# Kernel optimization log

Hardware: AMD Instinct MI355X
Metric: run time of the kernel (lower is better)

Reference implementation:

```python
import jax, jax.numpy as jnp
import numpy as np
import math

B, S, HID = 1, 2048, 4096
HQ, HKV, D = 32, 8, 128
G = HQ // HKV          # GQA group size
OBS, W, SINK = 128, 32, 2
THETA = 500000.0
TOP_FRAC, MID_SPARSITY, LOW_FRAC = 0.05, 0.7, 0.20
K_KEEP = int(math.ceil((1.0 - MID_SPARSITY) * D))  # elements kept per level-1 token


def _rope(x):
    # x: [B, H, S, D]; standard Llama rotary embedding
    half = D // 2
    inv_freq = 1.0 / (THETA ** (jnp.arange(half, dtype=jnp.float32) / half))
    ang = jnp.arange(S, dtype=jnp.float32)[:, None] * inv_freq[None, :]  # [S, half]
    cos = jnp.concatenate([jnp.cos(ang), jnp.cos(ang)], axis=-1)  # [S, D]
    sin = jnp.concatenate([jnp.sin(ang), jnp.sin(ang)], axis=-1)
    x1, x2 = x[..., :half], x[..., half:]
    rot = jnp.concatenate([-x2, x1], axis=-1)
    return x * cos[None, None] + rot * sin[None, None]


def _topk_mask(x):
    # keep the K_KEEP largest-magnitude elements of each length-D token vector
    a = jnp.abs(x)
    thr = jnp.sort(a, axis=-1)[..., D - K_KEEP]
    return a >= thr[..., None]


def setup_inputs() -> dict:
    key = jax.random.key(0)
    ks = jax.random.split(key, 5)
    sc = HID ** -0.5
    return {
        "hidden_states": jax.random.normal(ks[0], (B, S, HID), dtype=jnp.float32),
        "wq": jax.random.normal(ks[1], (HID, HQ * D), dtype=jnp.float32) * sc,
        "wk": jax.random.normal(ks[2], (HID, HKV * D), dtype=jnp.float32) * sc,
        "wv": jax.random.normal(ks[3], (HID, HKV * D), dtype=jnp.float32) * sc,
        "wo": jax.random.normal(ks[4], (HQ * D, HID), dtype=jnp.float32) * sc,
    }


def reference(hidden_states, wq, wk, wv, wo):
    scale = 1.0 / math.sqrt(D)
    q = (hidden_states @ wq).reshape(B, S, HQ, D).transpose(0, 2, 1, 3)   # [B,HQ,S,D]
    k = (hidden_states @ wk).reshape(B, S, HKV, D).transpose(0, 2, 1, 3)  # [B,HKV,S,D]
    v = (hidden_states @ wv).reshape(B, S, HKV, D).transpose(0, 2, 1, 3)
    q, k = _rope(q), _rope(k)

    # --- observation-window GQA attention (grouped queries vs all keys) ---
    obs_q = q[:, :, S - OBS:, :].reshape(B, HKV, G, OBS, D)
    s_obs = jnp.einsum('bhgqd,bhkd->bhgqk', obs_q, k) * scale
    obs_causal = jnp.arange(S)[None, :] <= (S - OBS + jnp.arange(OBS))[:, None]  # [OBS,S]
    s_obs = jnp.where(obs_causal[None, None, None], s_obs, -jnp.inf)
    aw_kv = jax.nn.softmax(s_obs.astype(jnp.float32), axis=-1).mean(axis=2)  # [B,HKV,OBS,S]

    # per-token importance, normalized by how many obs queries observed each key
    counts = jnp.minimum(OBS, S - jnp.arange(S)).astype(jnp.float32)
    imp = aw_kv.sum(axis=2) / counts[None, None, :]  # [B,HKV,S]

    # --- global thresholds over the compressible region -> 3 sparsity levels ---
    imp_c = imp[:, :, :S - W].reshape(-1)
    t_high = jnp.quantile(imp_c, 1.0 - TOP_FRAC)
    t_low = jnp.quantile(imp_c, LOW_FRAC)
    level = jnp.where(imp >= t_high, 0, jnp.where(imp < t_low, 2, 1))
    pos = jnp.arange(S)
    dense_pos = (pos >= S - W) | (pos < SINK)     # recent window + sinks stay dense
    level = jnp.where(dense_pos[None, None, :], 0, level)

    keep_k = jnp.where((level == 0)[..., None], True, (level == 1)[..., None] & _topk_mask(k))
    keep_v = jnp.where((level == 0)[..., None], True, (level == 1)[..., None] & _topk_mask(v))
    k_sp = k * keep_k
    v_sp = v * keep_v
    evicted = level == 2

    # --- causal GQA attention over the sparsified KV cache ---
    q_g = q.reshape(B, HKV, G, S, D)
    s = jnp.einsum('bhgqd,bhkd->bhgqk', q_g, k_sp) * scale
    causal = jnp.tril(jnp.ones((S, S), dtype=bool))
    allow = causal[None, None, None] & (~evicted)[:, :, None, None, :]
    s = jnp.where(allow, s, -jnp.inf)
    p = jax.nn.softmax(s.astype(jnp.float32), axis=-1).astype(v_sp.dtype)
    o = jnp.einsum('bhgqk,bhkd->bhgqd', p, v_sp)
    o = o.reshape(B, HQ, S, D).transpose(0, 2, 1, 3).reshape(B, S, HQ * D)
    return o @ wo
```

## Files before the change

### kernel.cpp

```cpp
#include <hip/hip_runtime.h>
#include <hip/hip_bf16.h>
#include <math.h>

#define S_    2048
#define HID_  4096
#define HQ_   32
#define HKV_  8
#define D_    128
#define G_    4
#define OBS_  128
#define W_    32
#define NKV_  1024
#define NQ_   4096
#define KLD_  2048
#define SCALE_ 0.08838834764831845f
#define THR_IDX_ 89
#define NC_   16128

typedef __attribute__((ext_vector_type(4))) float f32x4;
typedef __attribute__((ext_vector_type(8))) short s16x8;
typedef __attribute__((ext_vector_type(8))) unsigned short u16x8;
typedef __attribute__((ext_vector_type(4))) unsigned short u16x4;
typedef unsigned short ushort_t;

struct TermPtrs { const ushort_t* a[6]; const ushort_t* b[6]; };

__device__ __forceinline__ unsigned short f2bf(float x) {
  union { float f; unsigned u; } v; v.f = x;
  unsigned r = v.u + 0x7FFFu + ((v.u >> 16) & 1u);
  return (unsigned short)(r >> 16);
}
__device__ __forceinline__ float bf2f(unsigned short b) {
  union { unsigned u; float f; } v; v.u = ((unsigned)b) << 16;
  return v.f;
}
__device__ __forceinline__ void gload_lds16(const void* g, void* l) {
  __builtin_amdgcn_global_load_lds((const __attribute__((address_space(1))) unsigned int*)g,
                                   (__attribute__((address_space(3))) unsigned int*)l, 16, 0, 0);
}
__device__ __forceinline__ void term_sel(const TermPtrs& P, int tt,
                                         const ushort_t*& As, const ushort_t*& Bs) {
  switch (tt) {
    case 0: As = P.a[0]; Bs = P.b[0]; break;
    case 1: As = P.a[1]; Bs = P.b[1]; break;
    case 2: As = P.a[2]; Bs = P.b[2]; break;
    case 3: As = P.a[3]; Bs = P.b[3]; break;
    case 4: As = P.a[4]; Bs = P.b[4]; break;
    default: As = P.a[5]; Bs = P.b[5]; break;
  }
}
__device__ __forceinline__ void xcd_bmbn(int& bm, int& bn) {
  int nplane = gridDim.x * gridDim.y;
  int l = blockIdx.y * gridDim.x + blockIdx.x;
  int v = (l & 7) * (nplane >> 3) + (l >> 3);
  bm = v / gridDim.x;
  bn = v - bm * gridDim.x;
}

__global__ __launch_bounds__(256) void split3_kernel(const float* __restrict__ src,
                                                     ushort_t* __restrict__ d0,
                                                     ushort_t* __restrict__ d1,
                                                     ushort_t* __restrict__ d2, int n4) {
  int idx = blockIdx.x * 256 + threadIdx.x;
  if (idx >= n4) return;
  float4 v = ((const float4*)src)[idx];
  u16x4 o0, o1, o2;
  float xs[4] = {v.x, v.y, v.z, v.w};
#pragma unroll
  for (int e = 0; e < 4; ++e) {
    float x = xs[e];
    unsigned short b0 = f2bf(x);
    float r = x - bf2f(b0);
    unsigned short b1 = f2bf(r);
    o0[e] = b0; o1[e] = b1; o2[e] = f2bf(r - bf2f(b1));
  }
  *(u16x4*)(d0 + (size_t)idx * 4) = o0;
  *(u16x4*)(d1 + (size_t)idx * 4) = o1;
  *(u16x4*)(d2 + (size_t)idx * 4) = o2;
}

__global__ __launch_bounds__(256) void splitT_kernel(const float* __restrict__ src, int N,
                                                     ushort_t* __restrict__ t0,
                                                     ushort_t* __restrict__ t1,
                                                     ushort_t* __restrict__ t2) {
  __shared__ float tile[64][65];
  const int t = threadIdx.x;
  const int n0 = blockIdx.x * 64, k0 = blockIdx.y * 64;
#pragma unroll
  for (int i = 0; i < 16; ++i) {
    int idx = i * 256 + t;
    int r = idx >> 6, c = idx & 63;
    tile[r][c] = src[(size_t)(k0 + r) * N + n0 + c];
  }
  __syncthreads();
#pragma unroll
  for (int i = 0; i < 16; ++i) {
    int idx = i * 256 + t;
    int n = idx >> 6, kk = idx & 63;
    float x = tile[kk][n];
    unsigned short b0 = f2bf(x);
    size_t o = (size_t)(n0 + n) * HID_ + k0 + kk;
    t0[o] = b0;
    if (t1) {
      float r = x - bf2f(b0);
      unsigned short b1 = f2bf(r);
      t1[o] = b1;
      t2[o] = f2bf(r - bf2f(b1));
    }
  }
}

template<int TPZ>
__global__ __launch_bounds__(256) void gemm6(TermPtrs P, float* __restrict__ Cbase,
                                             int M, int N, int K) {
  __shared__ ushort_t lds[2 * 128 * 64];
  const int t = threadIdx.x;
  const int wave = t >> 6, lane = t & 63;
  const int lc = lane & 15, lg = lane >> 4;
  int bm, bn;
  xcd_bmbn(bm, bn);
  const int z = blockIdx.z;
  const int wm = wave >> 1, wn = wave & 1;
  const int srow = t >> 3, schunk = t & 7;
  float* C = Cbase + (size_t)z * M * N;

  f32x4 acc[4][4];
#pragma unroll
  for (int fi = 0; fi < 4; ++fi)
#pragma unroll
    for (int fj = 0; fj < 4; ++fj) acc[fi][fj] = 0.f;

  for (int tt = z * TPZ; tt < z * TPZ + TPZ; ++tt) {
    const ushort_t *As, *Bs;
    term_sel(P, tt, As, Bs);
    for (int kb = 0; kb < K / 64; ++kb) {
      __syncthreads();
#pragma unroll
      for (int g = 0; g < 4; ++g) {
        int row = g * 32 + srow;
        int sw = schunk ^ (row & 7);
        gload_lds16(As + (size_t)(bm * 128 + row) * K + kb * 64 + sw * 8,
                    lds + g * 2048 + wave * 512);
        gload_lds16(Bs + (size_t)(bn * 128 + row) * K + kb * 64 + sw * 8,
                    lds + 8192 + g * 2048 + wave * 512);
      }
      __syncthreads();
#pragma unroll
      for (int ks = 0; ks < 2; ++ks) {
        s16x8 af[4], bf[4];
#pragma unroll
        for (int f = 0; f < 4; ++f) {
          int ra = wm * 64 + f * 16 + lc;
          af[f] = *(const s16x8*)(lds + ra * 64 + (((ks * 4 + lg) ^ (ra & 7)) * 8));
          int rb = wn * 64 + f * 16 + lc;
          bf[f] = *(const s16x8*)(lds + 8192 + rb * 64 + (((ks * 4 + lg) ^ (rb & 7)) * 8));
        }
#pragma unroll
        for (int fi = 0; fi < 4; ++fi)
#pragma unroll
          for (int fj = 0; fj < 4; ++fj)
            acc[fi][fj] = __builtin_amdgcn_mfma_f32_16x16x32_bf16(af[fi], bf[fj], acc[fi][fj], 0, 0, 0);
      }
    }
  }
#pragma unroll
  for (int fi = 0; fi < 4; ++fi)
#pragma unroll
    for (int fj = 0; fj < 4; ++fj)
#pragma unroll
      for (int r = 0; r < 4; ++r)
        C[(size_t)(bm * 128 + wm * 64 + fi * 16 + lg * 4 + r) * N +
          bn * 128 + wn * 64 + fj * 16 + lc] = acc[fi][fj][r];
}

__global__ __launch_bounds__(256) void gemm1(const ushort_t* __restrict__ A,
                                             const ushort_t* __restrict__ B,
                                             float* __restrict__ Cbase,
                                             int M, int N, int K, int KSTEPS) {
  __shared__ ushort_t lds[2 * 128 * 64];
  const int t = threadIdx.x;
  const int wave = t >> 6, lane = t & 63;
  const int lc = lane & 15, lg = lane >> 4;
  int bm, bn;
  xcd_bmbn(bm, bn);
  const int z = blockIdx.z;
  const int wm = wave >> 1, wn = wave & 1;
  const int srow = t >> 3, schunk = t & 7;
  float* C = Cbase + (size_t)z * M * N;

  f32x4 acc[4][4];
#pragma unroll
  for (int fi = 0; fi < 4; ++fi)
#pragma unroll
    for (int fj = 0; fj < 4; ++fj) acc[fi][fj] = 0.f;

  for (int kb = z * KSTEPS; kb < z * KSTEPS + KSTEPS; ++kb) {
    __syncthreads();
#pragma unroll
    for (int g = 0; g < 4; ++g) {
      int row = g * 32 + srow;
      int sw = schunk ^ (row & 7);
      size_t co = kb * 64 + sw * 8;
      gload_lds16(A + (size_t)(bm * 128 + row) * K + co, lds + g * 2048 + wave * 512);
      gload_lds16(B + (size_t)(bn * 128 + row) * K + co, lds + 8192 + g * 2048 + wave * 512);
    }
    __syncthreads();
#pragma unroll
    for (int ks = 0; ks < 2; ++ks) {
      s16x8 af[4], bf[4];
#pragma unroll
      for (int f = 0; f < 4; ++f) {
        int ra = wm * 64 + f * 16 + lc;
        af[f] = *(const s16x8*)(lds + ra * 64 + (((ks * 4 + lg) ^ (ra & 7)) * 8));
        int rb = wn * 64 + f * 16 + lc;
        bf[f] = *(const s16x8*)(lds + 8192 + rb * 64 + (((ks * 4 + lg) ^ (rb & 7)) * 8));
      }
#pragma unroll
      for (int fi = 0; fi < 4; ++fi)
#pragma unroll
        for (int fj = 0; fj < 4; ++fj)
          acc[fi][fj] = __builtin_amdgcn_mfma_f32_16x16x32_bf16(af[fi], bf[fj], acc[fi][fj], 0, 0, 0);
    }
  }
#pragma unroll
  for (int fi = 0; fi < 4; ++fi)
#pragma unroll
    for (int fj = 0; fj < 4; ++fj)
#pragma unroll
      for (int r = 0; r < 4; ++r)
        C[(size_t)(bm * 128 + wm * 64 + fi * 16 + lg * 4 + r) * N +
          bn * 128 + wn * 64 + fj * 16 + lc] = acc[fi][fj][r];
}

__global__ __launch_bounds__(256) void gemm6k(TermPtrs P, float* __restrict__ Cp, int N) {
  __shared__ ushort_t lds[2 * 128 * 64];
  const int t = threadIdx.x;
  const int wave = t >> 6, lane = t & 63;
  const int lc = lane & 15, lg = lane >> 4;
  const int bn = blockIdx.x, z = blockIdx.z;
  const int wm = wave >> 1, wn = wave & 1;
  const int srow = t >> 3, schunk = t & 7;
  float* C = Cp + (size_t)z * 128 * N;

  f32x4 acc[4][4];
#pragma unroll
  for (int fi = 0; fi < 4; ++fi)
#pragma unroll
    for (int fj = 0; fj < 4; ++fj) acc[fi][fj] = 0.f;

  for (int tt = 0; tt < 6; ++tt) {
    const ushort_t *As, *Bs;
    term_sel(P, tt, As, Bs);
    for (int kb = z * 8; kb < z * 8 + 8; ++kb) {
      __syncthreads();
#pragma unroll
      for (int g = 0; g < 4; ++g) {
        int row = g * 32 + srow;
        int sw = schunk ^ (row & 7);
        gload_lds16(As + (size_t)row * HID_ + kb * 64 + sw * 8,
                    lds + g * 2048 + wave * 512);
        gload_lds16(Bs + (size_t)(bn * 128 + row) * HID_ + kb * 64 + sw * 8,
                    lds + 8192 + g * 2048 + wave * 512);
      }
      __syncthreads();
#pragma unroll
      for (int ks = 0; ks < 2; ++ks) {
        s16x8 af[4], bf[4];
#pragma unroll
        for (int f = 0; f < 4; ++f) {
          int ra = wm * 64 + f * 16 + lc;
          af[f] = *(const s16x8*)(lds + ra * 64 + (((ks * 4 + lg) ^ (ra & 7)) * 8));
          int rb = wn * 64 + f * 16 + lc;
          bf[f] = *(const s16x8*)(lds + 8192 + rb * 64 + (((ks * 4 + lg) ^ (rb & 7)) * 8));
        }
#pragma unroll
        for (int fi = 0; fi < 4; ++fi)
#pragma unroll
          for (int fj = 0; fj < 4; ++fj)
            acc[fi][fj] = __builtin_amdgcn_mfma_f32_16x16x32_bf16(af[fi], bf[fj], acc[fi][fj], 0, 0, 0);
      }
    }
  }
#pragma unroll
  for (int fi = 0; fi < 4; ++fi)
#pragma unroll
    for (int fj = 0; fj < 4; ++fj)
#pragma unroll
      for (int r = 0; r < 4; ++r)
        C[(size_t)(wm * 64 + fi * 16 + lg * 4 + r) * N +
          bn * 128 + wn * 64 + fj * 16 + lc] = acc[fi][fj][r];
}

__global__ __launch_bounds__(256) void gemm6z(TermPtrs P, float* __restrict__ Cg) {
  __shared__ ushort_t lds[2 * 128 * 64];
  const int t = threadIdx.x;
  const int wave = t >> 6, lane = t & 63;
  const int lc = lane & 15, lg = lane >> 4;
  const int bm = blockIdx.y, bn = blockIdx.x, z = blockIdx.z;
  const int wm = wave >> 1, wn = wave & 1;
  const int srow = t >> 3, schunk = t & 7;
  const size_t Aoff = (size_t)z * 512 * 128;
  const size_t Boff = (size_t)z * 2048 * 128;
  float* C = Cg + (size_t)z * 512 * 2048;

  f32x4 acc[4][4];
#pragma unroll
  for (int fi = 0; fi < 4; ++fi)
#pragma unroll
    for (int fj = 0; fj < 4; ++fj) acc[fi][fj] = 0.f;

  for (int tt = 0; tt < 6; ++tt) {
    const ushort_t *As, *Bs;
    term_sel(P, tt, As, Bs);
    As += Aoff; Bs += Boff;
    for (int kb = 0; kb < 2; ++kb) {
      __syncthreads();
#pragma unroll
      for (int g = 0; g < 4; ++g) {
        int row = g * 32 + srow;
        int sw = schunk ^ (row & 7);
        gload_lds16(As + (size_t)(bm * 128 + row) * 128 + kb * 64 + sw * 8,
                    lds + g * 2048 + wave * 512);
        gload_lds16(Bs + (size_t)(bn * 128 + row) * 128 + kb * 64 + sw * 8,
                    lds + 8192 + g * 2048 + wave * 512);
      }
      __syncthreads();
#pragma unroll
      for (int ks = 0; ks < 2; ++ks) {
        s16x8 af[4], bf[4];
#pragma unroll
        for (int f = 0; f < 4; ++f) {
          int ra = wm * 64 + f * 16 + lc;
          af[f] = *(const s16x8*)(lds + ra * 64 + (((ks * 4 + lg) ^ (ra & 7)) * 8));
          int rb = wn * 64 + f * 16 + lc;
          bf[f] = *(const s16x8*)(lds + 8192 + rb * 64 + (((ks * 4 + lg) ^ (rb & 7)) * 8));
        }
#pragma unroll
        for (int fi = 0; fi < 4; ++fi)
#pragma unroll
          for (int fj = 0; fj < 4; ++fj)
            acc[fi][fj] = __builtin_amdgcn_mfma_f32_16x16x32_bf16(af[fi], bf[fj], acc[fi][fj], 0, 0, 0);
      }
    }
  }
#pragma unroll
  for (int fi = 0; fi < 4; ++fi)
#pragma unroll
    for (int fj = 0; fj < 4; ++fj)
#pragma unroll
      for (int r = 0; r < 4; ++r)
        C[(size_t)(bm * 128 + wm * 64 + fi * 16 + lg * 4 + r) * 2048 +
          bn * 128 + wn * 64 + fj * 16 + lc] = acc[fi][fj][r];
}

__global__ void reduce3_kernel(const float* __restrict__ p, float* __restrict__ out, int n4) {
  int idx = blockIdx.x * 256 + threadIdx.x;
  if (idx >= n4) return;
  const size_t n = (size_t)n4 * 4;
  float4 a = ((const float4*)p)[idx];
  float4 b = ((const float4*)(p + n))[idx];
  float4 c = ((const float4*)(p + 2 * n))[idx];
  float4 o;
  o.x = a.x + b.x + c.x; o.y = a.y + b.y + c.y;
  o.z = a.z + b.z + c.z; o.w = a.w + b.w + c.w;
  ((float4*)out)[idx] = o;
}
__global__ void reduce2_kernel(const float* __restrict__ p, float* __restrict__ out, int n4) {
  int idx = blockIdx.x * 256 + threadIdx.x;
  if (idx >= n4) return;
  const size_t n = (size_t)n4 * 4;
  float4 a = ((const float4*)p)[idx];
  float4 b = ((const float4*)(p + n))[idx];
  float4 o;
  o.x = a.x + b.x; o.y = a.y + b.y; o.z = a.z + b.z; o.w = a.w + b.w;
  ((float4*)out)[idx] = o;
}

__global__ void freq_kernel(float* __restrict__ invf) {
  int j = threadIdx.x;
  if (j < 64) invf[j] = (float)(1.0 / pow(500000.0, (double)j / 64.0));
}

__global__ __launch_bounds__(256) void qobs_fuse(const float* __restrict__ qpart,
                                                 const float* __restrict__ invf,
                                                 ushort_t* __restrict__ q0,
                                                 ushort_t* __restrict__ q1,
                                                 ushort_t* __restrict__ q2) {
  int idx = blockIdx.x * 256 + threadIdx.x;
  int j = idx & 63;
  int hq = (idx >> 6) & 31;
  int i = idx >> 11;
  size_t base = (size_t)i * NQ_ + hq * 128 + j;
  float x1 = 0.f, x2 = 0.f;
#pragma unroll
  for (int z = 0; z < 8; ++z) {
    x1 += qpart[(size_t)z * OBS_ * NQ_ + base];
    x2 += qpart[(size_t)z * OBS_ * NQ_ + base + 64];
  }
  float ang = (float)(S_ - OBS_ + i) * invf[j];
  float sn, cs; sincosf(ang, &sn, &cs);
  float o1 = x1 * cs - x2 * sn;
  float o2 = x2 * cs + x1 * sn;
  int hk = hq >> 2, g = hq & 3;
  size_t o = (size_t)hk * 65536 + (size_t)(g * 128 + i) * 128 + j;
  float ys[2] = {o1, o2};
#pragma unroll
  for (int e = 0; e < 2; ++e) {
    float x = ys[e];
    unsigned short b0 = f2bf(x);
    float r = x - bf2f(b0);
    unsigned short b1 = f2bf(r);
    q0[o + e * 64] = b0; q1[o + e * 64] = b1; q2[o + e * 64] = f2bf(r - bf2f(b1));
  }
}

__global__ __launch_bounds__(256) void ropekv_splitk(float* __restrict__ kvf,
                                                     const float* __restrict__ invf,
                                                     ushort_t* __restrict__ k0,
                                                     ushort_t* __restrict__ k1,
                                                     ushort_t* __restrict__ k2) {
  int idx = blockIdx.x * 256 + threadIdx.x;
  int j = idx & 63;
  int h = (idx >> 6) & 7;
  int s = idx >> 9;
  size_t base = (size_t)s * KLD_ + h * 128 + j;
  float x1 = kvf[base], x2 = kvf[base + 64];
  float ang = (float)s * invf[j];
  float sn, cs; sincosf(ang, &sn, &cs);
  float o1 = x1 * cs - x2 * sn;
  float o2 = x2 * cs + x1 * sn;
  kvf[base] = o1; kvf[base + 64] = o2;
  size_t o = (size_t)h * 262144 + (size_t)s * 128 + j;
  float ys[2] = {o1, o2};
#pragma unroll
  for (int e = 0; e < 2; ++e) {
    float x = ys[e];
    unsigned short b0 = f2bf(x);
    float r = x - bf2f(b0);
    unsigned short b1 = f2bf(r);
    k0[o + e * 64] = b0; k1[o + e * 64] = b1; k2[o + e * 64] = f2bf(r - bf2f(b1));
  }
}

__global__ __launch_bounds__(256) void rope_q_fuse(const float* __restrict__ qp,
                                                   const float* __restrict__ invf,
                                                   ushort_t* __restrict__ qb16) {
  int idx = blockIdx.x * 256 + threadIdx.x;
  int j = idx & 63;
  int h = (idx >> 6) & 31;
  int s = idx >> 11;
  size_t base = (size_t)s * NQ_ + h * 128 + j;
  const size_t zs = (size_t)S_ * NQ_;
  float x1 = qp[base] + qp[base + zs];
  float x2 = qp[base + 64] + qp[base + 64 + zs];
  float ang = (float)s * invf[j];
  float sn, cs; sincosf(ang, &sn, &cs);
  qb16[base] = f2bf(x1 * cs - x2 * sn);
  qb16[base + 64] = f2bf(x2 * cs + x1 * sn);
}

__global__ __launch_bounds__(256) void rowstat_kernel(const float* __restrict__ s,
                                                      float* __restrict__ mx,
                                                      float* __restrict__ dinv) {
  const int row = blockIdx.x * 4 + (threadIdx.x >> 6);
  const int lane = threadIdx.x & 63;
  const int i = row & 127;
  const int jmax = S_ - OBS_ + i;
  const float* sp = s + (size_t)row * S_;
  float vals[32];
  float m = -INFINITY;
#pragma unroll
  for (int c = 0; c < 8; ++c) {
    int j0 = c * 256 + lane * 4;
    float4 v = *(const float4*)(sp + j0);
    float e0 = (j0 + 0 <= jmax) ? v.x * SCALE_ : -INFINITY;
    float e1 = (j0 + 1 <= jmax) ? v.y * SCALE_ : -INFINITY;
    float e2 = (j0 + 2 <= jmax) ? v.z * SCALE_ : -INFINITY;
    float e3 = (j0 + 3 <= jmax) ? v.w * SCALE_ : -INFINITY;
    vals[c * 4 + 0] = e0; vals[c * 4 + 1] = e1; vals[c * 4 + 2] = e2; vals[c * 4 + 3] = e3;
    m = fmaxf(m, fmaxf(fmaxf(e0, e1), fmaxf(e2, e3)));
  }
#pragma unroll
  for (int off = 1; off < 64; off <<= 1) m = fmaxf(m, __shfl_xor(m, off, 64));
  float ssum = 0.f;
#pragma unroll
  for (int c = 0; c < 32; ++c) ssum += expf(vals[c] - m);
#pragma unroll
  for (int off = 1; off < 64; off <<= 1) ssum += __shfl_xor(ssum, off, 64);
  if (lane == 0) { mx[row] = m; dinv[row] = 1.0f / ssum; }
}

__global__ __launch_bounds__(256) void colsum_part(const float* __restrict__ s,
                                                   const float* __restrict__ mx,
                                                   const float* __restrict__ dinv,
                                                   float* __restrict__ part) {
  __shared__ float mxl[64], dvl[64];
  const int jt = blockIdx.x, hk = blockIdx.y, rc = blockIdx.z;
  const int t = threadIdx.x;
  if (t < 64) {
    mxl[t] = mx[hk * 512 + rc * 64 + t];
    dvl[t] = dinv[hk * 512 + rc * 64 + t];
  }
  __syncthreads();
  const int j = jt * 256 + t;
  const float* sp = s + ((size_t)hk * 512 + rc * 64) * S_ + j;
  float acc = 0.f;
  for (int rr = 0; rr < 64; ++rr) {
    int i = (rc * 64 + rr) & 127;
    if (j <= S_ - OBS_ + i)
      acc += expf(sp[(size_t)rr * S_] * SCALE_ - mxl[rr]) * dvl[rr];
  }
  part[((size_t)rc * 8 + hk) * S_ + j] = acc;
}

__global__ void colsum_fin(const float* __restrict__ part, float* __restrict__ imp) {
  int idx = blockIdx.x * 256 + threadIdx.x;
  int hk = idx >> 11, j = idx & 2047;
  float acc = 0.f;
#pragma unroll
  for (int rc = 0; rc < 8; ++rc) acc += part[((size_t)rc * 8 + hk) * S_ + j];
  float cnt = (float)min(OBS_, S_ - j);
  imp[idx] = acc * 0.25f / cnt;
}

__global__ __launch_bounds__(1024) void radix_all(const float* __restrict__ imp,
                                                  float* __restrict__ thr) {
  __shared__ unsigned hist[4][256];
  __shared__ unsigned pfx_s[4], need_s[4];
  const int t = threadIdx.x;
  if (t < 4) {
    pfx_s[t] = 0u;
    need_s[t] = (t == 0) ? 3225u : (t == 1) ? 3226u : (t == 2) ? 15320u : 15321u;
  }
  __syncthreads();
  for (int pass = 0; pass < 4; ++pass) {
    ((unsigned*)hist)[t] = 0u;
    __syncthreads();
    int shift = 24 - pass * 8;
    for (int idx = t; idx < NC_; idx += 1024) {
      int h = idx / (S_ - W_), j = idx - h * (S_ - W_);
      union { float f; unsigned u; } cv; cv.f = imp[h * S_ + j];
      unsigned u = cv.u;
#pragma unroll
      for (int q = 0; q < 4; ++q) {
        bool m = (pass == 0) || ((u >> (shift + 8)) == (pfx_s[q] >> (shift + 8)));
        if (m) atomicAdd(&hist[q][(u >> shift) & 255u], 1u);
      }
    }
    __syncthreads();
    if (t < 4) {
      unsigned need = need_s[t], cum = 0, pfx = pfx_s[t];
      for (int d = 0; d < 256; ++d) {
        unsigned c = hist[t][d];
        if (cum + c > need) { pfx |= ((unsigned)d) << shift; need_s[t] = need - cum; break; }
        cum += c;
      }
      pfx_s[t] = pfx;
    }
    __syncthreads();
  }
  if (t == 0) {
    union { unsigned u; float f; } c0, c1, c2, c3;
    c0.u = pfx_s[0]; c1.u = pfx_s[1]; c2.u = pfx_s[2]; c3.u = pfx_s[3];
    double fl = 0.2 * (double)(NC_ - 1) - 3225.0;
    double fh = 0.95 * (double)(NC_ - 1) - 15320.0;
    thr[0] = (float)((double)c2.f + ((double)c3.f - (double)c2.f) * fh);
    thr[1] = (float)((double)c0.f + ((double)c1.f - (double)c0.f) * fl);
  }
}

__global__ __launch_bounds__(128) void sparsify_kernel(const float* __restrict__ kv,
                                                       const float* __restrict__ imp,
                                                       const float* __restrict__ thr,
                                                       ushort_t* __restrict__ ksp,
                                                       ushort_t* __restrict__ vsp,
                                                       float* __restrict__ ebias) {
  const int b = blockIdx.x;
  const int j = b >> 3;
  const int h = b & 7;
  const int t = threadIdx.x;
  float ipv = imp[h * S_ + j];
  bool dense = (j >= S_ - W_) || (j < 2);
  int lvl = dense ? 0 : ((ipv >= thr[0]) ? 0 : ((ipv < thr[1]) ? 2 : 1));
  if (t == 0) ebias[h * S_ + j] = (lvl == 2) ? -INFINITY : 0.0f;
  __shared__ float av[128];
  __shared__ float thv;
  size_t base_in = (size_t)j * KLD_ + h * D_;
  size_t base_out = (size_t)j * NKV_ + h * D_;
  float kvv = kv[base_in + t];
  av[t] = fabsf(kvv);
  __syncthreads();
  {
    float at = av[t]; int cnt = 0;
    for (int m = 0; m < 128; ++m) { float am = av[m]; cnt += (am < at) || (am == at && m < t); }
    if (cnt == THR_IDX_) thv = at;
  }
  __syncthreads();
  {
    bool keep = (lvl == 0) || (lvl == 1 && fabsf(kvv) >= thv);
    ksp[base_out + t] = f2bf(keep ? kvv : 0.0f);
  }
  __syncthreads();
  float vvv = kv[base_in + 1024 + t];
  av[t] = fabsf(vvv);
  __syncthreads();
  {
    float at = av[t]; int cnt = 0;
    for (int m = 0; m < 128; ++m) { float am = av[m]; cnt += (am < at) || (am == at && m < t); }
    if (cnt == THR_IDX_) thv = at;
  }
  __syncthreads();
  {
    bool keep = (lvl == 0) || (lvl == 1 && fabsf(vvv) >= thv);
    vsp[base_out + t] = f2bf(keep ? vvv : 0.0f);
  }
}

__global__ __launch_bounds__(256) void vtrans_kernel(const ushort_t* __restrict__ vsp,
                                                     ushort_t* __restrict__ vspT) {
  __shared__ ushort_t tl[64][136];
  const int jt = blockIdx.x;
  const int hk = blockIdx.y;
  const int t = threadIdx.x;
#pragma unroll
  for (int i = 0; i < 4; ++i) {
    int idx = i * 256 + t;
    int j = idx >> 4, c = idx & 15;
    *(u16x8*)&tl[j][c * 8] = *(const u16x8*)(vsp + (size_t)(jt * 64 + j) * NKV_ + hk * 128 + c * 8);
  }
  __syncthreads();
  int d = t >> 1, j0 = (t & 1) * 32;
#pragma unroll
  for (int jj = 0; jj < 4; ++jj) {
    u16x8 v;
#pragma unroll
    for (int e = 0; e < 8; ++e) v[e] = tl[j0 + jj * 8 + e][d];
    *(u16x8*)(vspT + ((size_t)hk * 128 + d) * S_ + jt * 64 + j0 + jj * 8) = v;
  }
}

#define SPAD_ 66
__global__ __launch_bounds__(256) void attn_kernel(const ushort_t* __restrict__ qbp,
                                                   const ushort_t* __restrict__ ksp,
                                                   const ushort_t* __restrict__ vspT,
                                                   const float* __restrict__ ebias,
                                                   ushort_t* __restrict__ ob16) {
  __shared__ ushort_t k_lds[64 * 128];
  __shared__ ushort_t vT_lds[128 * 64];
  __shared__ float s_lds[4][16][SPAD_];
  const int b = blockIdx.x;
  const int xcd = b & 7;
  const int idx = b >> 3;
  const int h = xcd * 4 + (idx >> 4);
  const int p = idx & 15;
  const int hk = h >> 2;
  const int t = threadIdx.x;
  const int w = t >> 6, lane = t & 63;
  const int lc = lane & 15, lg = lane >> 4;

  const ushort_t* kbase = ksp + hk * D_;
  const ushort_t* vbase = vspT + (size_t)hk * D_ * S_;

  for (int strip = 0; strip < 2; ++strip) {
    const int qb = (strip == 0) ? p : 31 - p;
    const int q0 = qb * 64 + w * 16;
    s16x8 qfrag[4];
#pragma unroll
    for (int db = 0; db < 4; ++db)
      qfrag[db] = *(const s16x8*)(qbp + (size_t)(q0 + lc) * NQ_ + h * D_ + db * 32 + lg * 8);

    f32x4 o[8];
#pragma unroll
    for (int n = 0; n < 8; ++n) o[n] = 0.f;
    float mr[4] = {-INFINITY, -INFINITY, -INFINITY, -INFINITY};
    float lr[4] = {0.f, 0.f, 0.f, 0.f};

    const int ntj = qb + 1;
    for (int tj = 0; tj < ntj; ++tj) {
      const int j0 = tj * 64;
      __syncthreads();
#pragma unroll
      for (int i = 0; i < 4; ++i) {
        int slot = i * 256 + w * 64 + lane;
        int row = slot >> 4, c = slot & 15;
        const ushort_t* gp = kbase + (size_t)(j0 + row) * NKV_ + ((c ^ (row & 7)) * 8);
        gload_lds16(gp, &k_lds[(i * 256 + w * 64) * 8]);
      }
#pragma unroll
      for (int i = 0; i < 4; ++i) {
        int slot = i * 256 + w * 64 + lane;
        int d = slot >> 3, c = slot & 7;
        const ushort_t* gp = vbase + (size_t)d * S_ + j0 + ((c ^ (d & 7)) * 8);
        gload_lds16(gp, &vT_lds[(i * 256 + w * 64) * 8]);
      }
      __syncthreads();

      f32x4 sfr[4];
#pragma unroll
      for (int js = 0; js < 4; ++js) sfr[js] = 0.f;
#pragma unroll
      for (int js = 0; js < 4; ++js) {
        int row = js * 16 + lc;
#pragma unroll
        for (int db = 0; db < 4; ++db) {
          s16x8 kf = *(const s16x8*)&k_lds[row * 128 + (((db * 4 + lg) ^ (lc & 7)) * 8)];
          sfr[js] = __builtin_amdgcn_mfma_f32_16x16x32_bf16(qfrag[db], kf, sfr[js], 0, 0, 0);
        }
      }
      float eb[4];
#pragma unroll
      for (int js = 0; js < 4; ++js) eb[js] = ebias[hk * S_ + j0 + js * 16 + lc];

      const bool diag = (tj == qb);
      float sclv[4];
#pragma unroll
      for (int r = 0; r < 4; ++r) {
        float sv[4];
#pragma unroll
        for (int js = 0; js < 4; ++js) sv[js] = sfr[js][r] * SCALE_ + eb[js];
        if (diag) {
          int qrow = w * 16 + lg * 4 + r;
#pragma unroll
          for (int js = 0; js < 4; ++js)
            if (js * 16 + lc > qrow) sv[js] = -INFINITY;
        }
        float tm = fmaxf(fmaxf(sv[0], sv[1]), fmaxf(sv[2], sv[3]));
#pragma unroll
        for (int off = 1; off < 16; off <<= 1) tm = fmaxf(tm, __shfl_xor(tm, off, 64));
        float mnew = fmaxf(mr[r], tm);
        float scl = __expf(mr[r] - mnew);
        float ps = 0.f;
#pragma unroll
        for (int js = 0; js < 4; ++js) {
          float e = __expf(sv[js] - mnew);
          s_lds[w][lg * 4 + r][js * 16 + lc] = e;
          ps += e;
        }
#pragma unroll
        for (int off = 1; off < 16; off <<= 1) ps += __shfl_xor(ps, off, 64);
        lr[r] = lr[r] * scl + ps;
        mr[r] = mnew;
        sclv[r] = scl;
      }
#pragma unroll
      for (int n = 0; n < 8; ++n) {
        f32x4 ov = o[n];
#pragma unroll
        for (int r = 0; r < 4; ++r) ov[r] *= sclv[r];
        o[n] = ov;
      }
      asm volatile("s_waitcnt lgkmcnt(0)" ::: "memory");
      s16x8 pa[2];
#pragma unroll
      for (int ks = 0; ks < 2; ++ks) {
        float pv[8];
        *(f32x4*)&pv[0] = *(const f32x4*)&s_lds[w][lc][ks * 32 + lg * 8];
        *(f32x4*)&pv[4] = *(const f32x4*)&s_lds[w][lc][ks * 32 + lg * 8 + 4];
        s16x8 pk;
#pragma unroll
        for (int e = 0; e < 8; ++e) pk[e] = (short)f2bf(pv[e]);
        pa[ks] = pk;
      }
#pragma unroll
      for (int n = 0; n < 8; ++n) {
        int d = n * 16 + lc;
#pragma unroll
        for (int ks = 0; ks < 2; ++ks) {
          s16x8 vf = *(const s16x8*)&vT_lds[d * 64 + (((ks * 4 + lg) ^ (lc & 7)) * 8)];
          o[n] = __builtin_amdgcn_mfma_f32_16x16x32_bf16(pa[ks], vf, o[n], 0, 0, 0);
        }
      }
    }
#pragma unroll
    for (int r = 0; r < 4; ++r) {
      float rinv = 1.0f / lr[r];
      int row = q0 + lg * 4 + r;
#pragma unroll
      for (int n = 0; n < 8; ++n)
        ob16[(size_t)row * NQ_ + h * D_ + n * 16 + lc] = f2bf(o[n][r] * rinv);
    }
  }
}

extern "C" void kernel_launch(void* const* d_in, const int* in_sizes, int n_in,
                              void* d_out, int out_size, void* d_ws, size_t ws_size,
                              hipStream_t stream) {
  (void)in_sizes; (void)n_in; (void)out_size; (void)ws_size;
  const float* hid = (const float*)d_in[0];
  const float* wq  = (const float*)d_in[1];
  const float* wk  = (const float*)d_in[2];
  const float* wv  = (const float*)d_in[3];
  const float* wo  = (const float*)d_in[4];
  float* out = (float*)d_out;
  char* ws = (char*)d_ws;
  const size_t MB = 1ull << 20;

  ushort_t* h0     = (ushort_t*)(ws + 0 * MB);
  ushort_t* h1     = (ushort_t*)(ws + 16 * MB);
  ushort_t* h2     = (ushort_t*)(ws + 32 * MB);
  ushort_t* wq0T   = (ushort_t*)(ws + 48 * MB);
  ushort_t* wq1T   = (ushort_t*)(ws + 80 * MB);
  ushort_t* wq2T   = (ushort_t*)(ws + 112 * MB);
  ushort_t* wkv0T  = (ushort_t*)(ws + 144 * MB);
  ushort_t* wkv1T  = (ushort_t*)(ws + 160 * MB);
  ushort_t* wkv2T  = (ushort_t*)(ws + 176 * MB);
  float*    qpart  = (float*)(ws + 192 * MB);
  float*    kvf    = (float*)(ws + 192 * MB);
  float*    kvp    = (float*)(ws + 80 * MB);
  float*    qp2    = (float*)(ws + 80 * MB);
  ushort_t* qb16   = (ushort_t*)(ws + 16 * MB);
  ushort_t* kb0    = (ushort_t*)(ws + 32 * MB);
  ushort_t* kb1    = (ushort_t*)(ws + 36 * MB);
  ushort_t* kb2    = (ushort_t*)(ws + 40 * MB);
  float*    s_obs  = (float*)(ws + 48 * MB);
  ushort_t* woT    = (ushort_t*)(ws + 144 * MB);
  ushort_t* ksp    = (ushort_t*)(ws + 176 * MB);
  ushort_t* vsp    = (ushort_t*)(ws + 180 * MB);
  ushort_t* vspT   = (ushort_t*)(ws + 184 * MB);
  ushort_t* ob16   = (ushort_t*)(ws + 188 * MB + 512 * 1024);
  float*    opart  = (float*)(ws + 0 * MB);
  ushort_t* qo0    = (ushort_t*)(ws + 208 * MB);
  ushort_t* qo1    = (ushort_t*)(ws + 209 * MB);
  ushort_t* qo2    = (ushort_t*)(ws + 210 * MB);
  char*     misc   = ws + 212 * MB;
  float*    impv   = (float*)(misc + 0);
  float*    eb     = (float*)(misc + 64 * 1024);
  float*    invf   = (float*)(misc + 128 * 1024);
  float*    thr    = (float*)(misc + 132 * 1024);
  float*    mxbuf  = (float*)(misc + 160 * 1024);
  float*    dinvb  = (float*)(misc + 192 * 1024);
  float*    part   = (float*)(misc + 256 * 1024);

  freq_kernel<<<1, 64, 0, stream>>>(invf);

  split3_kernel<<<(S_ * HID_ / 4 + 255) / 256, 256, 0, stream>>>(hid, h0, h1, h2, S_ * HID_ / 4);
  splitT_kernel<<<dim3(NQ_ / 64, HID_ / 64), 256, 0, stream>>>(wq, NQ_, wq0T, wq1T, wq2T);
  splitT_kernel<<<dim3(NKV_ / 64, HID_ / 64), 256, 0, stream>>>(wk, NKV_, wkv0T, wkv1T, wkv2T);
  splitT_kernel<<<dim3(NKV_ / 64, HID_ / 64), 256, 0, stream>>>(
      wv, NKV_, wkv0T + (size_t)NKV_ * HID_, wkv1T + (size_t)NKV_ * HID_, wkv2T + (size_t)NKV_ * HID_);

  const size_t obs_off = (size_t)(S_ - OBS_) * HID_;
  {
    TermPtrs P;
    P.a[0] = h0 + obs_off; P.b[0] = wq0T;
    P.a[1] = h0 + obs_off; P.b[1] = wq1T;
    P.a[2] = h1 + obs_off; P.b[2] = wq0T;
    P.a[3] = h1 + obs_off; P.b[3] = wq1T;
    P.a[4] = h0 + obs_off; P.b[4] = wq2T;
    P.a[5] = h2 + obs_off; P.b[5] = wq0T;
    gemm6k<<<dim3(NQ_ / 128, 1, 8), 256, 0, stream>>>(P, qpart, NQ_);
  }
  qobs_fuse<<<(OBS_ * HQ_ * 64) / 256, 256, 0, stream>>>(qpart, invf, qo0, qo1, qo2);

  {
    TermPtrs P;
    P.a[0] = h0; P.b[0] = wkv0T;
    P.a[1] = h0; P.b[1] = wkv1T;
    P.a[2] = h1; P.b[2] = wkv0T;
    P.a[3] = h1; P.b[3] = wkv1T;
    P.a[4] = h0; P.b[4] = wkv2T;
    P.a[5] = h2; P.b[5] = wkv0T;
    gemm6<2><<<dim3(KLD_ / 128, S_ / 128, 3), 256, 0, stream>>>(P, kvp, S_, KLD_, HID_);
  }
  reduce3_kernel<<<(S_ * KLD_ / 4 + 255) / 256, 256, 0, stream>>>(kvp, kvf, S_ * KLD_ / 4);

  gemm1<<<dim3(NQ_ / 128, S_ / 128, 2), 256, 0, stream>>>(h0, wq0T, qp2, S_, NQ_, HID_, 32);

  splitT_kernel<<<dim3(HID_ / 64, HID_ / 64), 256, 0, stream>>>(wo, HID_, woT, nullptr, nullptr);

  rope_q_fuse<<<(S_ * HQ_ * 64) / 256, 256, 0, stream>>>(qp2, invf, qb16);
  ropekv_splitk<<<(S_ * HKV_ * 64) / 256, 256, 0, stream>>>(kvf, invf, kb0, kb1, kb2);

  {
    TermPtrs P;
    P.a[0] = qo0; P.b[0] = kb0;
    P.a[1] = qo0; P.b[1] = kb1;
    P.a[2] = qo1; P.b[2] = kb0;
    P.a[3] = qo1; P.b[3] = kb1;
    P.a[4] = qo0; P.b[4] = kb2;
    P.a[5] = qo2; P.b[5] = kb0;
    gemm6z<<<dim3(16, 4, 8), 256, 0, stream>>>(P, s_obs);
  }
  rowstat_kernel<<<1024, 256, 0, stream>>>(s_obs, mxbuf, dinvb);
  colsum_part<<<dim3(8, 8, 8), 256, 0, stream>>>(s_obs, mxbuf, dinvb, part);
  colsum_fin<<<64, 256, 0, stream>>>(part, impv);

  radix_all<<<1, 1024, 0, stream>>>(impv, thr);

  sparsify_kernel<<<S_ * HKV_, 128, 0, stream>>>(kvf, impv, thr, ksp, vsp, eb);
  vtrans_kernel<<<dim3(S_ / 64, HKV_), 256, 0, stream>>>(vsp, vspT);
  attn_kernel<<<512, 256, 0, stream>>>(qb16, ksp, vspT, eb, ob16);
  gemm1<<<dim3(HID_ / 128, S_ / 128, 2), 256, 0, stream>>>(ob16, woT, opart, S_, HID_, HID_, 32);
  reduce2_kernel<<<(S_ * HID_ / 4 + 255) / 256, 256, 0, stream>>>(opart, out, S_ * HID_ / 4);
}
```

Before: 974.9 us.

## Fuse six split-bf16 GEMM terms into one K-loop sharing loaded tiles

```diff
diff --git a/kernel.cpp b/kernel.cpp
--- a/kernel.cpp
+++ b/kernel.cpp
@@ -24,6 +24,7 @@
 typedef unsigned short ushort_t;
 
 struct TermPtrs { const ushort_t* a[6]; const ushort_t* b[6]; };
+struct Six { const ushort_t* A[3]; const ushort_t* B[3]; };
 
 __device__ __forceinline__ unsigned short f2bf(float x) {
   union { float f; unsigned u; } v; v.f = x;
@@ -110,10 +111,9 @@
   }
 }
 
-template<int TPZ>
-__global__ __launch_bounds__(256) void gemm6(TermPtrs P, float* __restrict__ Cbase,
-                                             int M, int N, int K) {
-  __shared__ ushort_t lds[2 * 128 * 64];
+__global__ __launch_bounds__(256) void gemm6s(Six P, float* __restrict__ Cbase,
+                                              int M, int N, int K, int KSTEPS) {
+  __shared__ ushort_t lds[6 * 128 * 32];
   const int t = threadIdx.x;
   const int wave = t >> 6, lane = t & 63;
   const int lc = lane & 15, lg = lane >> 4;
@@ -121,7 +121,6 @@
   xcd_bmbn(bm, bn);
   const int z = blockIdx.z;
   const int wm = wave >> 1, wn = wave & 1;
-  const int srow = t >> 3, schunk = t & 7;
   float* C = Cbase + (size_t)z * M * N;
 
   f32x4 acc[4][4];
@@ -130,38 +129,66 @@
 #pragma unroll
     for (int fj = 0; fj < 4; ++fj) acc[fi][fj] = 0.f;
 
-  for (int tt = z * TPZ; tt < z * TPZ + TPZ; ++tt) {
-    const ushort_t *As, *Bs;
-    term_sel(P, tt, As, Bs);
-    for (int kb = 0; kb < K / 64; ++kb) {
-      __syncthreads();
-#pragma unroll
-      for (int g = 0; g < 4; ++g) {
-        int row = g * 32 + srow;
-        int sw = schunk ^ (row & 7);
-        gload_lds16(As + (size_t)(bm * 128 + row) * K + kb * 64 + sw * 8,
-                    lds + g * 2048 + wave * 512);
-        gload_lds16(Bs + (size_t)(bn * 128 + row) * K + kb * 64 + sw * 8,
-                    lds + 8192 + g * 2048 + wave * 512);
-      }
-      __syncthreads();
-#pragma unroll
-      for (int ks = 0; ks < 2; ++ks) {
-        s16x8 af[4], bf[4];
-#pragma unroll
-        for (int f = 0; f < 4; ++f) {
-          int ra = wm * 64 + f * 16 + lc;
-          af[f] = *(const s16x8*)(lds + ra * 64 + (((ks * 4 + lg) ^ (ra & 7)) * 8));
-          int rb = wn * 64 + f * 16 + lc;
-          bf[f] = *(const s16x8*)(lds + 8192 + rb * 64 + (((ks * 4 + lg) ^ (rb & 7)) * 8));
-        }
-#pragma unroll
-        for (int fi = 0; fi < 4; ++fi)
-#pragma unroll
-          for (int fj = 0; fj < 4; ++fj)
-            acc[fi][fj] = __builtin_amdgcn_mfma_f32_16x16x32_bf16(af[fi], bf[fj], acc[fi][fj], 0, 0, 0);
-      }
-    }
+  for (int kb = z * KSTEPS; kb < z * KSTEPS + KSTEPS; ++kb) {
+    __syncthreads();
+#pragma unroll
+    for (int ti = 0; ti < 6; ++ti) {
+      const ushort_t* src = (ti < 3) ? P.A[ti] : P.B[ti - 3];
+      const int rb = ((ti < 3) ? bm : bn) * 128;
+#pragma unroll
+      for (int it = 0; it < 2; ++it) {
+        int slot = it * 256 + t;
+        int row = slot >> 2, c = slot & 3;
+        int sw = c ^ (row & 3);
+        gload_lds16(src + (size_t)(rb + row) * K + kb * 32 + sw * 8,
+                    lds + ti * 4096 + it * 2048 + wave * 512);
+      }
+    }
+    __syncthreads();
+    s16x8 a0[4], a1[4], a2[4], bfr[4];
+#pragma unroll
+    for (int f = 0; f < 4; ++f) {
+      int ra = wm * 64 + f * 16 + lc;
+      int ca = (lg ^ (ra & 3)) * 8;
+      a0[f] = *(const s16x8*)(lds + 0 * 4096 + ra * 32 + ca);
+      a1[f] = *(const s16x8*)(lds + 1 * 4096 + ra * 32 + ca);
+      a2[f] = *(const s16x8*)(lds + 2 * 4096 + ra * 32 + ca);
+    }
+#pragma unroll
+    for (int f = 0; f < 4; ++f) {
+      int rb2 = wn * 64 + f * 16 + lc;
+      bfr[f] = *(const s16x8*)(lds + 3 * 4096 + rb2 * 32 + ((lg ^ (rb2 & 3)) * 8));
+    }
+#pragma unroll
+    for (int fi = 0; fi < 4; ++fi)
+#pragma unroll
+      for (int fj = 0; fj < 4; ++fj) {
+        acc[fi][fj] = __builtin_amdgcn_mfma_f32_16x16x32_bf16(a0[fi], bfr[fj], acc[fi][fj], 0, 0, 0);
+        acc[fi][fj] = __builtin_amdgcn_mfma_f32_16x16x32_bf16(a1[fi], bfr[fj], acc[fi][fj], 0, 0, 0);
+        acc[fi][fj] = __builtin_amdgcn_mfma_f32_16x16x32_bf16(a2[fi], bfr[fj], acc[fi][fj], 0, 0, 0);
+      }
+#pragma unroll
+    for (int f = 0; f < 4; ++f) {
+      int rb2 = wn * 64 + f * 16 + lc;
+      bfr[f] = *(const s16x8*)(lds + 4 * 4096 + rb2 * 32 + ((lg ^ (rb2 & 3)) * 8));
+    }
+#pragma unroll
+    for (int fi = 0; fi < 4; ++fi)
+#pragma unroll
+      for (int fj = 0; fj < 4; ++fj) {
+        acc[fi][fj] = __builtin_amdgcn_mfma_f32_16x16x32_bf16(a0[fi], bfr[fj], acc[fi][fj], 0, 0, 0);
+        acc[fi][fj] = __builtin_amdgcn_mfma_f32_16x16x32_bf16(a1[fi], bfr[fj], acc[fi][fj], 0, 0, 0);
+      }
+#pragma unroll
+    for (int f = 0; f < 4; ++f) {
+      int rb2 = wn * 64 + f * 16 + lc;
+      bfr[f] = *(const s16x8*)(lds + 5 * 4096 + rb2 * 32 + ((lg ^ (rb2 & 3)) * 8));
+    }
+#pragma unroll
+    for (int fi = 0; fi < 4; ++fi)
+#pragma unroll
+      for (int fj = 0; fj < 4; ++fj)
+        acc[fi][fj] = __builtin_amdgcn_mfma_f32_16x16x32_bf16(a0[fi], bfr[fj], acc[fi][fj], 0, 0, 0);
   }
 #pragma unroll
   for (int fi = 0; fi < 4; ++fi)
@@ -232,65 +259,6 @@
           bn * 128 + wn * 64 + fj * 16 + lc] = acc[fi][fj][r];
 }
 
-__global__ __launch_bounds__(256) void gemm6k(TermPtrs P, float* __restrict__ Cp, int N) {
-  __shared__ ushort_t lds[2 * 128 * 64];
-  const int t = threadIdx.x;
-  const int wave = t >> 6, lane = t & 63;
-  const int lc = lane & 15, lg = lane >> 4;
-  const int bn = blockIdx.x, z = blockIdx.z;
-  const int wm = wave >> 1, wn = wave & 1;
-  const int srow = t >> 3, schunk = t & 7;
-  float* C = Cp + (size_t)z * 128 * N;
-
-  f32x4 acc[4][4];
-#pragma unroll
-  for (int fi = 0; fi < 4; ++fi)
-#pragma unroll
-    for (int fj = 0; fj < 4; ++fj) acc[fi][fj] = 0.f;
-
-  for (int tt = 0; tt < 6; ++tt) {
-    const ushort_t *As, *Bs;
-    term_sel(P, tt, As, Bs);
-    for (int kb = z * 8; kb < z * 8 + 8; ++kb) {
-      __syncthreads();
-#pragma unroll
-      for (int g = 0; g < 4; ++g) {
-        int row = g * 32 + srow;
-        int sw = schunk ^ (row & 7);
-        gload_lds16(As + (size_t)row * HID_ + kb * 64 + sw * 8,
-                    lds + g * 2048 + wave * 512);
-        gload_lds16(Bs + (size_t)(bn * 128 + row) * HID_ + kb * 64 + sw * 8,
-                    lds + 8192 + g * 2048 + wave * 512);
-      }
-      __syncthreads();
-#pragma unroll
-      for (int ks = 0; ks < 2; ++ks) {
-        s16x8 af[4], bf[4];
-#pragma unroll
-        for (int f = 0; f < 4; ++f) {
-          int ra = wm * 64 + f * 16 + lc;
-          af[f] = *(const s16x8*)(lds + ra * 64 + (((ks * 4 + lg) ^ (ra & 7)) * 8));
-          int rb = wn * 64 + f * 16 + lc;
-          bf[f] = *(const s16x8*)(lds + 8192 + rb * 64 + (((ks * 4 + lg) ^ (rb & 7)) * 8));
-        }
-#pragma unroll
-        for (int fi = 0; fi < 4; ++fi)
-#pragma unroll
-          for (int fj = 0; fj < 4; ++fj)
-            acc[fi][fj] = __builtin_amdgcn_mfma_f32_16x16x32_bf16(af[fi], bf[fj], acc[fi][fj], 0, 0, 0);
-      }
-    }
-  }
-#pragma unroll
-  for (int fi = 0; fi < 4; ++fi)
-#pragma unroll
-    for (int fj = 0; fj < 4; ++fj)
-#pragma unroll
-      for (int r = 0; r < 4; ++r)
-        C[(size_t)(wm * 64 + fi * 16 + lg * 4 + r) * N +
-          bn * 128 + wn * 64 + fj * 16 + lc] = acc[fi][fj][r];
-}
-
 __global__ __launch_bounds__(256) void gemm6z(TermPtrs P, float* __restrict__ Cg) {
   __shared__ ushort_t lds[2 * 128 * 64];
   const int t = threadIdx.x;
@@ -353,16 +321,17 @@
           bn * 128 + wn * 64 + fj * 16 + lc] = acc[fi][fj][r];
 }
 
-__global__ void reduce3_kernel(const float* __restrict__ p, float* __restrict__ out, int n4) {
+__global__ void reduce4_kernel(const float* __restrict__ p, float* __restrict__ out, int n4) {
   int idx = blockIdx.x * 256 + threadIdx.x;
   if (idx >= n4) return;
   const size_t n = (size_t)n4 * 4;
   float4 a = ((const float4*)p)[idx];
   float4 b = ((const float4*)(p + n))[idx];
   float4 c = ((const float4*)(p + 2 * n))[idx];
+  float4 d = ((const float4*)(p + 3 * n))[idx];
   float4 o;
-  o.x = a.x + b.x + c.x; o.y = a.y + b.y + c.y;
-  o.z = a.z + b.z + c.z; o.w = a.w + b.w + c.w;
+  o.x = a.x + b.x + c.x + d.x; o.y = a.y + b.y + c.y + d.y;
+  o.z = a.z + b.z + c.z + d.z; o.w = a.w + b.w + c.w + d.w;
   ((float4*)out)[idx] = o;
 }
 __global__ void reduce2_kernel(const float* __restrict__ p, float* __restrict__ out, int n4) {
@@ -841,28 +810,20 @@
 
   const size_t obs_off = (size_t)(S_ - OBS_) * HID_;
   {
-    TermPtrs P;
-    P.a[0] = h0 + obs_off; P.b[0] = wq0T;
-    P.a[1] = h0 + obs_off; P.b[1] = wq1T;
-    P.a[2] = h1 + obs_off; P.b[2] = wq0T;
-    P.a[3] = h1 + obs_off; P.b[3] = wq1T;
-    P.a[4] = h0 + obs_off; P.b[4] = wq2T;
-    P.a[5] = h2 + obs_off; P.b[5] = wq0T;
-    gemm6k<<<dim3(NQ_ / 128, 1, 8), 256, 0, stream>>>(P, qpart, NQ_);
+    Six P;
+    P.A[0] = h0 + obs_off; P.A[1] = h1 + obs_off; P.A[2] = h2 + obs_off;
+    P.B[0] = wq0T; P.B[1] = wq1T; P.B[2] = wq2T;
+    gemm6s<<<dim3(NQ_ / 128, 1, 8), 256, 0, stream>>>(P, qpart, 128, NQ_, HID_, 16);
   }
   qobs_fuse<<<(OBS_ * HQ_ * 64) / 256, 256, 0, stream>>>(qpart, invf, qo0, qo1, qo2);
 
   {
-    TermPtrs P;
-    P.a[0] = h0; P.b[0] = wkv0T;
-    P.a[1] = h0; P.b[1] = wkv1T;
-    P.a[2] = h1; P.b[2] = wkv0T;
-    P.a[3] = h1; P.b[3] = wkv1T;
-    P.a[4] = h0; P.b[4] = wkv2T;
-    P.a[5] = h2; P.b[5] = wkv0T;
-    gemm6<2><<<dim3(KLD_ / 128, S_ / 128, 3), 256, 0, stream>>>(P, kvp, S_, KLD_, HID_);
-  }
-  reduce3_kernel<<<(S_ * KLD_ / 4 + 255) / 256, 256, 0, stream>>>(kvp, kvf, S_ * KLD_ / 4);
+    Six P;
+    P.A[0] = h0; P.A[1] = h1; P.A[2] = h2;
+    P.B[0] = wkv0T; P.B[1] = wkv1T; P.B[2] = wkv2T;
+    gemm6s<<<dim3(KLD_ / 128, S_ / 128, 4), 256, 0, stream>>>(P, kvp, S_, KLD_, HID_, 32);
+  }
+  reduce4_kernel<<<(S_ * KLD_ / 4 + 255) / 256, 256, 0, stream>>>(kvp, kvf, S_ * KLD_ / 4);
 
   gemm1<<<dim3(NQ_ / 128, S_ / 128, 2), 256, 0, stream>>>(h0, wq0T, qp2, S_, NQ_, HID_, 32);
 
```

Measured after the change: 855.9 us. 12.2% less time.
